# Optimization experiments

Hardware: AMD Instinct MI355X
Metric: run time of the kernel (lower is better)

Reference implementation:

```python
import jax, jax.numpy as jnp
from jax import lax
import numpy as np

B = 8
NC = 80               # num_classes / cls_out_channels
SCORE_THR = 0.01      # test_cfg.score_thr
IOU_THR = 0.65        # test_cfg.nms.iou_threshold
PRE_TOPK = 5000       # min(num_bboxes, 5000)
MAX_PER_IMG = 100     # keepTopK
LEVELS = [(80, 80, 8), (40, 40, 16), (20, 20, 32)]  # (H, W, stride)


def make_priors():
    # MlvlPointGenerator with_stride=True: [x*s, y*s, s, s]
    parts = []
    for H, W, s in LEVELS:
        ys, xs = jnp.meshgrid(jnp.arange(H, dtype=jnp.float32),
                              jnp.arange(W, dtype=jnp.float32), indexing='ij')
        st = jnp.full((H * W,), float(s), dtype=jnp.float32)
        parts.append(jnp.stack([xs.ravel() * s, ys.ravel() * s, st, st], -1))
    return jnp.concatenate(parts, 0)  # [N, 4]


def _flatten(t, c):
    # NCHW -> [B, H*W, c]
    return t.transpose(0, 2, 3, 1).reshape(t.shape[0], -1, c)


def _decode(priors, bp):
    # priors [N,4], bp [B,N,4] -> xyxy boxes [B,N,4]
    xys = bp[..., :2] * priors[:, 2:] + priors[:, :2]
    whs = jnp.exp(bp[..., 2:]) * priors[:, 2:]
    return jnp.concatenate([xys - whs / 2, xys + whs / 2], -1)


def _iou_one(box, boxes):
    # box [4] vs boxes [T,4]
    tl = jnp.maximum(box[:2], boxes[:, :2])
    br = jnp.minimum(box[2:], boxes[:, 2:])
    wh = jnp.clip(br - tl, 0.0)
    inter = wh[:, 0] * wh[:, 1]
    a1 = (box[2] - box[0]) * (box[3] - box[1])
    a2 = (boxes[:, 2] - boxes[:, 0]) * (boxes[:, 3] - boxes[:, 1])
    return inter / (a1 + a2 - inter + 1e-6)


def _nms_single(boxes, scores):
    # greedy NMS on one class: boxes [T,4], scores [T]
    s0 = jnp.where(scores > SCORE_THR, scores, -1.0)

    def step(s, _):
        i = jnp.argmax(s)
        best = s[i]
        iou = _iou_one(boxes[i], boxes)
        s = jnp.where(iou > IOU_THR, -1.0, s).at[i].set(-1.0)
        return s, (i, jnp.where(best > 0, best, -1.0))

    _, (idx, ks) = lax.scan(jax.checkpoint(step), s0, None, length=MAX_PER_IMG)
    return idx, ks  # [K] indices into boxes, [K] kept scores (-1 = invalid)


def _per_image(boxes, scores):
    # boxes [N,4], scores [N,C]
    top_s, top_i = lax.top_k(scores.T, PRE_TOPK)          # [C,T]
    top_b = boxes[top_i]                                   # [C,T,4]
    idx, ks = jax.vmap(_nms_single)(top_b, top_s)          # [C,K]
    cb = jnp.take_along_axis(top_b, idx[..., None], axis=1)  # [C,K,4]
    cids = jnp.broadcast_to(jnp.arange(NC, dtype=jnp.int32)[:, None], ks.shape)
    fs, sel = lax.top_k(ks.reshape(-1), MAX_PER_IMG)       # global keepTopK
    fb = cb.reshape(-1, 4)[sel]
    fc = cids.reshape(-1)[sel]
    valid = fs > 0
    num = jnp.sum(valid.astype(jnp.int32))
    return (num,
            jnp.where(valid[:, None], fb, 0.0),
            jnp.where(valid, fs, 0.0),
            jnp.where(valid, fc, -1))


def _forward(cls0, bbox0, obj0, cls1, bbox1, obj1, cls2, bbox2, obj2):
    cls = jnp.concatenate([_flatten(c, NC) for c in (cls0, cls1, cls2)], 1)
    bp = jnp.concatenate([_flatten(b, 4) for b in (bbox0, bbox1, bbox2)], 1)
    obj = jnp.concatenate([_flatten(o, 1)[..., 0] for o in (obj0, obj1, obj2)], 1)
    priors = make_priors()
    boxes = _decode(priors, bp)                            # [B,N,4]
    scores = jax.nn.sigmoid(cls) * jax.nn.sigmoid(obj)[..., None]  # [B,N,C]
    return jax.vmap(_per_image)(boxes, scores)


def setup_inputs() -> dict:
    key = jax.random.key(0)
    ks = jax.random.split(key, 9)
    specs = [("cls0", (B, NC, 80, 80)), ("bbox0", (B, 4, 80, 80)), ("obj0", (B, 1, 80, 80)),
             ("cls1", (B, NC, 40, 40)), ("bbox1", (B, 4, 40, 40)), ("obj1", (B, 1, 40, 40)),
             ("cls2", (B, NC, 20, 20)), ("bbox2", (B, 4, 20, 20)), ("obj2", (B, 1, 20, 20))]
    return {n: jax.random.normal(k, sh, dtype=jnp.float32) for k, (n, sh) in zip(ks, specs)}


def reference(cls0, bbox0, obj0, cls1, bbox1, obj1, cls2, bbox2, obj2):
    # returns (num_detected [B], proposals [B,100,4], scores [B,100], cls_id [B,100])
    return _forward(cls0, bbox0, obj0, cls1, bbox1, obj1, cls2, bbox2, obj2)
```

## Files before the change

kernel.cpp:

```cpp
#include <hip/hip_runtime.h>
#include <math.h>
#include <stdint.h>

#define NCLS   80
#define NPTS   8400
#define KEEP   100
#define PRETOPK 5000
#define NB     8
#define THRBITS 0x3C23D70Au
#define BASEK   0x3C000000u

#define TBS    512
#define CAPF   448
#define NEEDF  192u
#define MTX    256
#define NW4    2100

#define TBT    1024
#define NREGT  8
#define CAPT   512

__device__ __forceinline__ float sigmoidf_(float x) { return 1.0f / (1.0f + expf(-x)); }

__device__ __forceinline__ float4 decode_one(int n, int b,
        const float* bb0, const float* bb1, const float* bb2) {
    const float* bb; int base, HW, x, y; float s;
    if (n < 6400)      { bb = bb0; base = n;        HW = 6400; s = 8.f;  y = base / 80; x = base - y * 80; }
    else if (n < 8000) { bb = bb1; base = n - 6400; HW = 1600; s = 16.f; y = base / 40; x = base - y * 40; }
    else               { bb = bb2; base = n - 8000; HW = 400;  s = 32.f; y = base / 20; x = base - y * 20; }
    const float* p = bb + (size_t)b * 4 * HW + base;
    float v0 = p[0], v1 = p[HW], v2 = p[2 * HW], v3 = p[3 * HW];
    float cx = v0 * s + x * s, cy = v1 * s + y * s;
    float w = expf(v2) * s, h = expf(v3) * s;
    return make_float4(cx - 0.5f * w, cy - 0.5f * h, cx + 0.5f * w, cy + 0.5f * h);
}

__device__ __forceinline__ bool iou_gt(float4 a, float4 c) {
    float tlx = fmaxf(a.x, c.x), tly = fmaxf(a.y, c.y);
    float brx = fminf(a.z, c.z), bry = fminf(a.w, c.w);
    float w = fmaxf(brx - tlx, 0.f), h = fmaxf(bry - tly, 0.f);
    float inter = w * h;
    float a1 = (a.z - a.x) * (a.w - a.y);
    float a2 = (c.z - c.x) * (c.w - c.y);
    return inter / (a1 + a2 - inter + 1e-6f) > 0.65f;
}

__device__ __forceinline__ void scan_hist1024(const uint32_t* sHist, uint32_t need, uint32_t cap,
                                              uint32_t carry, uint32_t prefix, int shift,
                                              uint32_t* shr, int lane) {
    const uint4* hv = (const uint4*)sHist;
    uint4 q0 = hv[lane * 4], q1 = hv[lane * 4 + 1], q2 = hv[lane * 4 + 2], q3 = hv[lane * 4 + 3];
    uint32_t csum = q0.x + q0.y + q0.z + q0.w + q1.x + q1.y + q1.z + q1.w
                  + q2.x + q2.y + q2.z + q2.w + q3.x + q3.y + q3.z + q3.w;
    uint32_t suf = csum;
    #pragma unroll
    for (int d = 1; d < 64; d <<= 1) {
        uint32_t t = (uint32_t)__shfl_down((int)suf, d);
        if (lane + d < 64) suf += t;
    }
    unsigned long long m = __ballot(carry + suf >= need);
    if (!m) { if (lane == 0) { shr[1] = 0u; shr[0] = 0u; } return; }
    int l1 = 63 - __clzll(m);
    uint32_t carry2 = carry + (uint32_t)__shfl((int)suf, l1) - (uint32_t)__shfl((int)csum, l1);
    uint32_t c2 = (lane < 16) ? sHist[l1 * 16 + lane] : 0u;
    uint32_t suf2 = c2;
    #pragma unroll
    for (int d = 1; d < 16; d <<= 1) {
        uint32_t t = (uint32_t)__shfl_down((int)suf2, d);
        if (lane + d < 16) suf2 += t;
    }
    unsigned long long m2 = __ballot(lane < 16 && (carry2 + suf2 >= need));
    int t2 = m2 ? (63 - __clzll(m2)) : 0;
    uint32_t suf2L = (uint32_t)__shfl((int)suf2, t2);
    uint32_t c2L   = (uint32_t)__shfl((int)c2, t2);
    int bin = l1 * 16 + t2;
    uint32_t cAbove = carry2 + suf2L - c2L;
    uint32_t cntIncl = cAbove + c2L;
    if (lane == 0) {
        if (cntIncl <= cap) { shr[1] = 0u; shr[0] = prefix | ((uint32_t)bin << shift); }
        else { shr[1] = 1u; shr[2] = prefix | ((uint32_t)bin << shift); shr[3] = cAbove; }
    }
}

__device__ __forceinline__ void scan_hist64_final(const uint32_t* sHist, uint32_t need, uint32_t cap,
                                                  uint32_t carry, uint32_t prefix,
                                                  uint32_t* shr, int lane) {
    uint32_t c2 = sHist[lane];
    uint32_t suf2 = c2;
    #pragma unroll
    for (int d = 1; d < 64; d <<= 1) {
        uint32_t t = (uint32_t)__shfl_down((int)suf2, d);
        if (lane + d < 64) suf2 += t;
    }
    unsigned long long m2 = __ballot(carry + suf2 >= need);
    int t2 = m2 ? (63 - __clzll(m2)) : 0;
    uint32_t suf2L = (uint32_t)__shfl((int)suf2, t2);
    uint32_t c2L   = (uint32_t)__shfl((int)c2, t2);
    uint32_t cAbove = carry + suf2L - c2L;
    uint32_t cntIncl = cAbove + c2L;
    if (lane == 0) {
        shr[1] = 0u;
        shr[0] = (cntIncl <= cap) ? (prefix | (uint32_t)t2)
                                  : ((prefix | (uint32_t)t2) + 1u);
    }
}

__global__ __launch_bounds__(1024)
void sig_obj(const float* __restrict__ o0, const float* __restrict__ o1, const float* __restrict__ o2,
             float* __restrict__ so) {
    int t = blockIdx.x * 1024 + threadIdx.x;
    if (t >= NB * NPTS) return;
    int b = t / NPTS, n = t - b * NPTS;
    float v;
    if (n < 6400)      v = o0[(size_t)b * 6400 + n];
    else if (n < 8000) v = o1[(size_t)b * 1600 + (n - 6400)];
    else               v = o2[(size_t)b * 400 + (n - 8000)];
    so[t] = 1.0f / (1.0f + expf(-v));
}

__global__ __launch_bounds__(TBS, 6)
void select_nms(const float* __restrict__ cls0, const float* __restrict__ bb0,
                const float* __restrict__ cls1, const float* __restrict__ bb1,
                const float* __restrict__ cls2, const float* __restrict__ bb2,
                const float* __restrict__ sigObj,
                float* __restrict__ keptScore, float4* __restrict__ keptBox) {
    __shared__ __align__(16) uint32_t sKey[NPTS];
    __shared__ __align__(16) char uMem[8192];
    __shared__ uint32_t sKeyS[CAPF];
    __shared__ uint16_t sIdxS[CAPF];
    __shared__ __align__(16) float4 bBoxS[CAPF];
    __shared__ uint32_t shr[4];
    __shared__ unsigned long long sh64;

    uint32_t* sHist = (uint32_t*)uMem;
    unsigned long long* cPack = (unsigned long long*)(uMem + 4096);
    typedef unsigned long long ull4[4];
    ull4* colM = (ull4*)uMem;

    int bc = blockIdx.x;
    int b = bc & 7;
    int c = bc >> 3;
    int tid = threadIdx.x, lane = tid & 63;

    sHist[tid] = 0; sHist[tid + TBS] = 0;
    __syncthreads();
    uint4* sKey4 = (uint4*)sKey;
    #pragma unroll
    for (int i = 0; i < 5; ++i) {
        int w = tid + i * TBS;
        if (w < NW4) {
            int n = w << 2;
            const float* cp;
            if (w < 1600)      cp = cls0 + ((size_t)b * NCLS + c) * 6400 + n;
            else if (w < 2000) cp = cls1 + ((size_t)b * NCLS + c) * 1600 + (n - 6400);
            else               cp = cls2 + ((size_t)b * NCLS + c) * 400 + (n - 8000);
            float4 cv = *(const float4*)cp;
            float4 so = *(const float4*)(sigObj + (size_t)b * NPTS + n);
            uint32_t k0 = __float_as_uint(sigmoidf_(cv.x) * so.x);
            uint32_t k1 = __float_as_uint(sigmoidf_(cv.y) * so.y);
            uint32_t k2 = __float_as_uint(sigmoidf_(cv.z) * so.z);
            uint32_t k3 = __float_as_uint(sigmoidf_(cv.w) * so.w);
            sKey4[w] = make_uint4(k0, k1, k2, k3);
            if (k0 > THRBITS) atomicAdd(&sHist[(k0 - BASEK) >> 16], 1u);
            if (k1 > THRBITS) atomicAdd(&sHist[(k1 - BASEK) >> 16], 1u);
            if (k2 > THRBITS) atomicAdd(&sHist[(k2 - BASEK) >> 16], 1u);
            if (k3 > THRBITS) atomicAdd(&sHist[(k3 - BASEK) >> 16], 1u);
        }
    }
    __syncthreads();

    uint32_t prefix = 0, carry = 0, Tsel = 0;
    const uint4* k4 = (const uint4*)sKey;
    for (int level = 0;; ++level) {
        if (tid < 64) {
            if (level < 2) scan_hist1024(sHist, NEEDF, CAPF, carry, prefix, level == 0 ? 16 : 6, shr, lane);
            else           scan_hist64_final(sHist, NEEDF, CAPF, carry, prefix, shr, lane);
        }
        __syncthreads();
        if (shr[1] == 0u) { Tsel = shr[0]; break; }
        prefix = shr[2]; carry = shr[3];
        int nl = level + 1;
        if (nl == 2) { if (tid < 64) sHist[tid] = 0; } else { sHist[tid] = 0; sHist[tid + TBS] = 0; }
        __syncthreads();
        #pragma unroll
        for (int i = 0; i < 5; ++i) {
            int w = tid + i * TBS;
            if (w < NW4) {
                uint4 q = k4[w];
                #pragma unroll
                for (int j = 0; j < 4; ++j) {
                    uint32_t k = (j == 0) ? q.x : (j == 1) ? q.y : (j == 2) ? q.z : q.w;
                    if (k > THRBITS) {
                        uint32_t kp = k - BASEK;
                        if (nl == 1) { if ((kp >> 16) == (prefix >> 16)) atomicAdd(&sHist[(kp >> 6) & 1023u], 1u); }
                        else         { if ((kp >> 6)  == (prefix >> 6))  atomicAdd(&sHist[kp & 63u], 1u); }
                    }
                }
            }
        }
        __syncthreads();
    }
    __syncthreads();
    if (tid == 0) shr[3] = 0u;
    __syncthreads();

    #pragma unroll
    for (int i = 0; i < 5; ++i) {
        int w = tid + i * TBS;
        if (w < NW4) {
            uint4 q = k4[w];
            int n = w << 2;
            #pragma unroll
            for (int j = 0; j < 4; ++j) {
                uint32_t k = (j == 0) ? q.x : (j == 1) ? q.y : (j == 2) ? q.z : q.w;
                if (k > THRBITS && (k - BASEK) >= Tsel) {
                    uint32_t s = atomicAdd(&shr[3], 1u);
                    if (s < CAPF) cPack[s] = ((unsigned long long)k << 32) | (uint32_t)(0xFFFFu - (n + j));
                }
            }
        }
    }
    __syncthreads();
    int cnt = (int)shr[3]; if (cnt > CAPF) cnt = CAPF;
    if (tid < 16) cPack[cnt + tid] = 0ull;
    __syncthreads();

    if (tid < ((cnt + 63) & ~63)) {
        bool h0 = tid < cnt;
        unsigned long long my = h0 ? cPack[tid] : 0ull;
        int r0 = 0;
        const ulonglong2* cp2 = (const ulonglong2*)cPack;
        int nb16 = (cnt + 15) >> 4;
        for (int jb = 0; jb < nb16; ++jb) {
            ulonglong2 p0 = cp2[jb * 8 + 0], p1 = cp2[jb * 8 + 1], p2 = cp2[jb * 8 + 2], p3 = cp2[jb * 8 + 3];
            ulonglong2 p4 = cp2[jb * 8 + 4], p5 = cp2[jb * 8 + 5], p6 = cp2[jb * 8 + 6], p7 = cp2[jb * 8 + 7];
            r0 += (p0.x > my) + (p0.y > my) + (p1.x > my) + (p1.y > my)
                + (p2.x > my) + (p2.y > my) + (p3.x > my) + (p3.y > my)
                + (p4.x > my) + (p4.y > my) + (p5.x > my) + (p5.y > my)
                + (p6.x > my) + (p6.y > my) + (p7.x > my) + (p7.y > my);
        }
        if (h0) {
            sKeyS[r0] = (uint32_t)(my >> 32);
            sIdxS[r0] = (uint16_t)(0xFFFFu - (uint32_t)(my & 0xFFFFu));
        }
    }
    __syncthreads();

    if (tid < cnt) bBoxS[tid] = decode_one(sIdxS[tid], b, bb0, bb1, bb2);
    __syncthreads();

    int lim = (cnt < MTX) ? cnt : MTX;
    #pragma unroll
    for (int pp = 0; pp < 2; ++pp) {
        int t2 = tid + pp * TBS;
        int cand = t2 & 255, rb = t2 >> 8;
        unsigned long long m = 0ull;
        if (cand < lim) {
            float4 bcx = bBoxS[cand];
            int j0 = rb << 6;
            #pragma unroll 8
            for (int jj = 0; jj < 64; ++jj)
                if (iou_gt(bBoxS[j0 + jj], bcx)) m |= 1ull << jj;
        }
        colM[cand][rb] = m;
    }
    __syncthreads();

    float4 kb0 = make_float4(0.f, 0.f, 0.f, 0.f), kb1 = kb0;
    float ks0 = -1.0f, ks1 = -1.0f;
    int K = 0;
    if (tid < 64) {
        __builtin_amdgcn_s_setprio(1);
        unsigned long long U0, U1, U2, U3;
        U0 = (lim >= 64) ? ~0ull : ((lim > 0) ? ((1ull << lim) - 1) : 0ull);
        U1 = (lim >= 128) ? ~0ull : ((lim > 64) ? ((1ull << (lim - 64)) - 1) : 0ull);
        U2 = (lim >= 192) ? ~0ull : ((lim > 128) ? ((1ull << (lim - 128)) - 1) : 0ull);
        U3 = (lim >= 256) ? ~0ull : ((lim > 192) ? ((1ull << (lim - 192)) - 1) : 0ull);
        int kIA = -1, kIB = -1;
        while (K < KEEP) {
            int i;
            if (U0) i = (int)__ffsll(U0) - 1;
            else if (U1) i = 64 + (int)__ffsll(U1) - 1;
            else if (U2) i = 128 + (int)__ffsll(U2) - 1;
            else if (U3) i = 192 + (int)__ffsll(U3) - 1;
            else break;
            ulonglong2 r01 = *(const ulonglong2*)&colM[i][0];
            ulonglong2 r23 = *(const ulonglong2*)&colM[i][2];
            if (i < 64)       U0 &= ~(1ull << i);
            else if (i < 128) U1 &= ~(1ull << (i - 64));
            else if (i < 192) U2 &= ~(1ull << (i - 128));
            else              U3 &= ~(1ull << (i - 192));
            U0 &= ~r01.x; U1 &= ~r01.y; U2 &= ~r23.x; U3 &= ~r23.y;
            if (K < 64) { if (lane == K) kIA = i; }
            else        { if (lane == K - 64) kIB = i; }
            K++;
        }
        if (kIA >= 0) { kb0 = bBoxS[kIA]; ks0 = __uint_as_float(sKeyS[kIA]); }
        if (kIB >= 0) { kb1 = bBoxS[kIB]; ks1 = __uint_as_float(sKeyS[kIB]); }
        for (int i = lim; i < cnt && K < KEEP; ++i) {
            float4 bx = bBoxS[i];
            bool sup = false;
            if (lane < K)      sup = iou_gt(bx, kb0);
            if (64 + lane < K) sup = sup || iou_gt(bx, kb1);
            if (!__any(sup ? 1 : 0)) {
                float sc = __uint_as_float(sKeyS[i]);
                if (K < 64) { if (lane == K)      { kb0 = bx; ks0 = sc; } }
                else        { if (lane == K - 64) { kb1 = bx; ks1 = sc; } }
                K++;
            }
        }
        __builtin_amdgcn_s_setprio(0);
        if (lane == 0) {
            shr[0] = (uint32_t)K;
            shr[1] = (uint32_t)cnt;
            shr[2] = (cnt > 0) ? sKeyS[cnt - 1] : 0xFFFFFFFFu;
            shr[3] = (cnt > 0) ? (uint32_t)sIdxS[cnt - 1] : 0xFFFFFFFFu;
        }
    }
    __syncthreads();
    int Kall = (int)shr[0]; int e = (int)shr[1];
    uint32_t cK = shr[2], cI = shr[3];

    if (Kall < KEEP && e < PRETOPK) {
        for (;;) {
            if (tid == 0) sh64 = 0ull;
            __syncthreads();
            unsigned long long best = 0ull;
            for (int i = 0; i < 17; ++i) {
                int n = tid + i * TBS;
                if (n < NPTS) {
                    uint32_t k = sKey[n];
                    if (k > THRBITS && (k < cK || (k == cK && (uint32_t)n > cI))) {
                        unsigned long long v = ((unsigned long long)k << 32) | (unsigned long long)(NPTS - 1 - n);
                        if (v > best) best = v;
                    }
                }
            }
            if (best) atomicMax(&sh64, best);
            __syncthreads();
            unsigned long long bv = sh64;
            if (bv == 0ull) break;
            uint32_t k = (uint32_t)(bv >> 32);
            int n = NPTS - 1 - (int)(bv & 0xFFFFFFFFull);
            if (tid < 64) {
                float4 bx = decode_one(n, b, bb0, bb1, bb2);
                bool sup = false;
                if (lane < K)      sup = iou_gt(bx, kb0);
                if (64 + lane < K) sup = sup || iou_gt(bx, kb1);
                if (!__any(sup ? 1 : 0)) {
                    float sc = __uint_as_float(k);
                    if (K < 64) { if (lane == K)      { kb0 = bx; ks0 = sc; } }
                    else        { if (lane == K - 64) { kb1 = bx; ks1 = sc; } }
                    K++;
                }
                if (lane == 0) shr[0] = (uint32_t)K;
            }
            __syncthreads();
            Kall = (int)shr[0];
            e++; cK = k; cI = (uint32_t)n;
            if (Kall >= KEEP || e >= PRETOPK) break;
        }
    }

    if (tid < 64) {
        int off = (b * NCLS + c) * KEEP;
        float4 z = make_float4(0.f, 0.f, 0.f, 0.f);
        keptScore[off + lane] = (lane < K) ? ks0 : -1.0f;
        keptBox[off + lane]   = (lane < K) ? kb0 : z;
        if (64 + lane < KEEP) {
            keptScore[off + 64 + lane] = (64 + lane < K) ? ks1 : -1.0f;
            keptBox[off + 64 + lane]   = (64 + lane < K) ? kb1 : z;
        }
    }
}

__global__ __launch_bounds__(TBT)
void topk_out(const float* __restrict__ keptScore, const float4* __restrict__ keptBox,
              float* __restrict__ out) {
    __shared__ __align__(16) uint32_t sHist[1024];
    __shared__ __align__(16) unsigned long long cPackT[CAPT + 16];
    __shared__ uint32_t sKeyS[CAPT];
    __shared__ uint16_t sIdxS[CAPT];
    __shared__ uint32_t shr[4];
    int b = blockIdx.x, tid = threadIdx.x, lane = tid & 63;
    const int TOT = NCLS * KEEP;

    uint32_t rKey[NREGT];
    #pragma unroll
    for (int i = 0; i < NREGT; ++i) {
        int n = tid + i * TBT;
        uint32_t key = 0u;
        if (n < TOT) {
            float s = keptScore[b * TOT + n];
            key = (s > 0.f) ? __float_as_uint(s) : 0u;
        }
        rKey[i] = key;
    }

    uint32_t prefix = 0, carry = 0, Tsel = 0;
    for (int level = 0;; ++level) {
        __syncthreads();
        if (level == 2) { if (tid < 64) sHist[tid] = 0; } else sHist[tid] = 0;
        __syncthreads();
        #pragma unroll
        for (int i = 0; i < NREGT; ++i) {
            uint32_t k = rKey[i];
            if (k > 0u) {
                uint32_t kp = k - BASEK;
                if (level == 0) atomicAdd(&sHist[kp >> 16], 1u);
                else if (level == 1) { if ((kp >> 16) == (prefix >> 16)) atomicAdd(&sHist[(kp >> 6) & 1023u], 1u); }
                else { if ((kp >> 6) == (prefix >> 6)) atomicAdd(&sHist[kp & 63u], 1u); }
            }
        }
        __syncthreads();
        if (tid < 64) {
            if (level < 2) scan_hist1024(sHist, (uint32_t)KEEP, (uint32_t)CAPT, carry, prefix, level == 0 ? 16 : 6, shr, lane);
            else           scan_hist64_final(sHist, (uint32_t)KEEP, (uint32_t)CAPT, carry, prefix, shr, lane);
        }
        __syncthreads();
        if (shr[1] == 0u) { Tsel = shr[0]; break; }
        prefix = shr[2]; carry = shr[3];
    }
    __syncthreads();
    if (tid == 0) shr[3] = 0u;
    __syncthreads();
    #pragma unroll
    for (int i = 0; i < NREGT; ++i) {
        uint32_t k = rKey[i];
        if (k > 0u && (k - BASEK) >= Tsel) {
            uint32_t s = atomicAdd(&shr[3], 1u);
            if (s < CAPT) cPackT[s] = ((unsigned long long)k << 32) | (uint32_t)(0xFFFFu - (tid + i * TBT));
        }
    }
    __syncthreads();
    int cnt = (int)shr[3]; if (cnt > CAPT) cnt = CAPT;
    if (tid < 16) cPackT[cnt + tid] = 0ull;
    __syncthreads();

    if (tid < ((cnt + 63) & ~63)) {
        bool h0 = tid < cnt;
        unsigned long long my = h0 ? cPackT[tid] : 0ull;
        int r0 = 0;
        const ulonglong2* cp2 = (const ulonglong2*)cPackT;
        int nb16 = (cnt + 15) >> 4;
        for (int jb = 0; jb < nb16; ++jb) {
            ulonglong2 p0 = cp2[jb * 8 + 0], p1 = cp2[jb * 8 + 1], p2 = cp2[jb * 8 + 2], p3 = cp2[jb * 8 + 3];
            ulonglong2 p4 = cp2[jb * 8 + 4], p5 = cp2[jb * 8 + 5], p6 = cp2[jb * 8 + 6], p7 = cp2[jb * 8 + 7];
            r0 += (p0.x > my) + (p0.y > my) + (p1.x > my) + (p1.y > my)
                + (p2.x > my) + (p2.y > my) + (p3.x > my) + (p3.y > my)
                + (p4.x > my) + (p4.y > my) + (p5.x > my) + (p5.y > my)
                + (p6.x > my) + (p6.y > my) + (p7.x > my) + (p7.y > my);
        }
        if (h0) {
            sKeyS[r0] = (uint32_t)(my >> 32);
            sIdxS[r0] = (uint16_t)(0xFFFFu - (uint32_t)(my & 0xFFFFu));
        }
    }
    __syncthreads();

    if (tid < KEEP) {
        bool valid = tid < cnt;
        int fi = valid ? (int)sIdxS[tid] : 0;
        float sc = valid ? __uint_as_float(sKeyS[tid]) : 0.f;
        float4 bx = valid ? keptBox[b * TOT + fi] : make_float4(0.f, 0.f, 0.f, 0.f);
        float cls = valid ? (float)(fi / KEEP) : -1.0f;
        float* boxOut = out + NB + (b * KEEP + tid) * 4;
        boxOut[0] = bx.x; boxOut[1] = bx.y; boxOut[2] = bx.z; boxOut[3] = bx.w;
        out[NB + NB * KEEP * 4 + b * KEEP + tid] = sc;
        out[NB + NB * KEEP * 4 + NB * KEEP + b * KEEP + tid] = cls;
    }
    if (tid == 0) out[b] = (float)((cnt < KEEP) ? cnt : KEEP);
}

extern "C" void kernel_launch(void* const* d_in, const int* in_sizes, int n_in,
                              void* d_out, int out_size, void* d_ws, size_t ws_size,
                              hipStream_t stream) {
    const float* cls0 = (const float*)d_in[0];
    const float* bb0  = (const float*)d_in[1];
    const float* obj0 = (const float*)d_in[2];
    const float* cls1 = (const float*)d_in[3];
    const float* bb1  = (const float*)d_in[4];
    const float* obj1 = (const float*)d_in[5];
    const float* cls2 = (const float*)d_in[6];
    const float* bb2  = (const float*)d_in[7];
    const float* obj2 = (const float*)d_in[8];
    float* out = (float*)d_out;

    char* ws = (char*)d_ws;
    float*  keptScore = (float*)(ws);
    float4* keptBox   = (float4*)(ws + 256000);
    float*  sigObj    = (float*)(ws + 1280000);

    sig_obj<<<(NB * NPTS + 1023) / 1024, 1024, 0, stream>>>(obj0, obj1, obj2, sigObj);
    select_nms<<<NB * NCLS, TBS, 0, stream>>>(cls0, bb0, cls1, bb1, cls2, bb2,
                                              sigObj, keptScore, keptBox);
    topk_out<<<NB, TBT, 0, stream>>>(keptScore, keptBox, out);
}
```

Baseline: 159.3 us.

## Fuse objectness sigmoid into select kernel, triangular IoU mask, register-cached NMS rows

Drops the separate sig_obj launch and computes the objectness sigmoid inline from the raw obj inputs inside select_nms, so the per-class blocks recompute it rather than reading a precomputed buffer. The IoU bitmask build now skips blocks that lie entirely at or below the diagonal and masks out lower-triangle bits, roughly halving the pairwise IoU work. The serial greedy NMS loop preloads the suppression mask rows into registers and fetches them with wave shuffles instead of LDS reads on each iteration. The trade-offs are extra exp work per class block and higher register pressure in the NMS wave.

```diff
diff --git a/kernel.cpp b/kernel.cpp
--- a/kernel.cpp
+++ b/kernel.cpp
@@ -105,24 +105,13 @@
     }
 }
 
-__global__ __launch_bounds__(1024)
-void sig_obj(const float* __restrict__ o0, const float* __restrict__ o1, const float* __restrict__ o2,
-             float* __restrict__ so) {
-    int t = blockIdx.x * 1024 + threadIdx.x;
-    if (t >= NB * NPTS) return;
-    int b = t / NPTS, n = t - b * NPTS;
-    float v;
-    if (n < 6400)      v = o0[(size_t)b * 6400 + n];
-    else if (n < 8000) v = o1[(size_t)b * 1600 + (n - 6400)];
-    else               v = o2[(size_t)b * 400 + (n - 8000)];
-    so[t] = 1.0f / (1.0f + expf(-v));
-}
-
 __global__ __launch_bounds__(TBS, 6)
 void select_nms(const float* __restrict__ cls0, const float* __restrict__ bb0,
+                const float* __restrict__ o0,
                 const float* __restrict__ cls1, const float* __restrict__ bb1,
+                const float* __restrict__ o1,
                 const float* __restrict__ cls2, const float* __restrict__ bb2,
-                const float* __restrict__ sigObj,
+                const float* __restrict__ o2,
                 float* __restrict__ keptScore, float4* __restrict__ keptBox) {
     __shared__ __align__(16) uint32_t sKey[NPTS];
     __shared__ __align__(16) char uMem[8192];
@@ -150,16 +139,16 @@
         int w = tid + i * TBS;
         if (w < NW4) {
             int n = w << 2;
-            const float* cp;
-            if (w < 1600)      cp = cls0 + ((size_t)b * NCLS + c) * 6400 + n;
-            else if (w < 2000) cp = cls1 + ((size_t)b * NCLS + c) * 1600 + (n - 6400);
-            else               cp = cls2 + ((size_t)b * NCLS + c) * 400 + (n - 8000);
+            const float* cp; const float* op;
+            if (w < 1600)      { cp = cls0 + ((size_t)b * NCLS + c) * 6400 + n;          op = o0 + (size_t)b * 6400 + n; }
+            else if (w < 2000) { cp = cls1 + ((size_t)b * NCLS + c) * 1600 + (n - 6400); op = o1 + (size_t)b * 1600 + (n - 6400); }
+            else               { cp = cls2 + ((size_t)b * NCLS + c) * 400 + (n - 8000);  op = o2 + (size_t)b * 400 + (n - 8000); }
             float4 cv = *(const float4*)cp;
-            float4 so = *(const float4*)(sigObj + (size_t)b * NPTS + n);
-            uint32_t k0 = __float_as_uint(sigmoidf_(cv.x) * so.x);
-            uint32_t k1 = __float_as_uint(sigmoidf_(cv.y) * so.y);
-            uint32_t k2 = __float_as_uint(sigmoidf_(cv.z) * so.z);
-            uint32_t k3 = __float_as_uint(sigmoidf_(cv.w) * so.w);
+            float4 ov = *(const float4*)op;
+            uint32_t k0 = __float_as_uint(sigmoidf_(cv.x) * sigmoidf_(ov.x));
+            uint32_t k1 = __float_as_uint(sigmoidf_(cv.y) * sigmoidf_(ov.y));
+            uint32_t k2 = __float_as_uint(sigmoidf_(cv.z) * sigmoidf_(ov.z));
+            uint32_t k3 = __float_as_uint(sigmoidf_(cv.w) * sigmoidf_(ov.w));
             sKey4[w] = make_uint4(k0, k1, k2, k3);
             if (k0 > THRBITS) atomicAdd(&sHist[(k0 - BASEK) >> 16], 1u);
             if (k1 > THRBITS) atomicAdd(&sHist[(k1 - BASEK) >> 16], 1u);
@@ -254,13 +243,14 @@
     for (int pp = 0; pp < 2; ++pp) {
         int t2 = tid + pp * TBS;
         int cand = t2 & 255, rb = t2 >> 8;
+        int j0 = rb << 6;
         unsigned long long m = 0ull;
-        if (cand < lim) {
+        if (cand < lim && j0 + 63 > cand) {
             float4 bcx = bBoxS[cand];
-            int j0 = rb << 6;
             #pragma unroll 8
             for (int jj = 0; jj < 64; ++jj)
                 if (iou_gt(bBoxS[j0 + jj], bcx)) m |= 1ull << jj;
+            if (j0 <= cand) m &= ~((2ull << (cand - j0)) - 1ull);
         }
         colM[cand][rb] = m;
     }
@@ -270,6 +260,11 @@
     float ks0 = -1.0f, ks1 = -1.0f;
     int K = 0;
     if (tid < 64) {
+        const ulonglong2* cm2 = (const ulonglong2*)colM;
+        ulonglong2 a01 = cm2[lane * 2 + 0],        a23 = cm2[lane * 2 + 1];
+        ulonglong2 b01 = cm2[(64 + lane) * 2 + 0],  b23 = cm2[(64 + lane) * 2 + 1];
+        ulonglong2 c01 = cm2[(128 + lane) * 2 + 0], c23 = cm2[(128 + lane) * 2 + 1];
+        ulonglong2 d01 = cm2[(192 + lane) * 2 + 0], d23 = cm2[(192 + lane) * 2 + 1];
         __builtin_amdgcn_s_setprio(1);
         unsigned long long U0, U1, U2, U3;
         U0 = (lim >= 64) ? ~0ull : ((lim > 0) ? ((1ull << lim) - 1) : 0ull);
@@ -284,13 +279,17 @@
             else if (U2) i = 128 + (int)__ffsll(U2) - 1;
             else if (U3) i = 192 + (int)__ffsll(U3) - 1;
             else break;
-            ulonglong2 r01 = *(const ulonglong2*)&colM[i][0];
-            ulonglong2 r23 = *(const ulonglong2*)&colM[i][2];
+            int src = i & 63;
+            unsigned long long s0, s1, s2, s3;
+            if (i < 64)       { s0 = __shfl(a01.x, src); s1 = __shfl(a01.y, src); s2 = __shfl(a23.x, src); s3 = __shfl(a23.y, src); }
+            else if (i < 128) { s0 = __shfl(b01.x, src); s1 = __shfl(b01.y, src); s2 = __shfl(b23.x, src); s3 = __shfl(b23.y, src); }
+            else if (i < 192) { s0 = __shfl(c01.x, src); s1 = __shfl(c01.y, src); s2 = __shfl(c23.x, src); s3 = __shfl(c23.y, src); }
+            else              { s0 = __shfl(d01.x, src); s1 = __shfl(d01.y, src); s2 = __shfl(d23.x, src); s3 = __shfl(d23.y, src); }
             if (i < 64)       U0 &= ~(1ull << i);
             else if (i < 128) U1 &= ~(1ull << (i - 64));
             else if (i < 192) U2 &= ~(1ull << (i - 128));
             else              U3 &= ~(1ull << (i - 192));
-            U0 &= ~r01.x; U1 &= ~r01.y; U2 &= ~r23.x; U3 &= ~r23.y;
+            U0 &= ~s0; U1 &= ~s1; U2 &= ~s2; U3 &= ~s3;
             if (K < 64) { if (lane == K) kIA = i; }
             else        { if (lane == K - 64) kIB = i; }
             K++;
@@ -489,10 +488,8 @@
     char* ws = (char*)d_ws;
     float*  keptScore = (float*)(ws);
     float4* keptBox   = (float4*)(ws + 256000);
-    float*  sigObj    = (float*)(ws + 1280000);
-
-    sig_obj<<<(NB * NPTS + 1023) / 1024, 1024, 0, stream>>>(obj0, obj1, obj2, sigObj);
-    select_nms<<<NB * NCLS, TBS, 0, stream>>>(cls0, bb0, cls1, bb1, cls2, bb2,
-                                              sigObj, keptScore, keptBox);
+
+    select_nms<<<NB * NCLS, TBS, 0, stream>>>(cls0, bb0, obj0, cls1, bb1, obj1,
+                                              cls2, bb2, obj2, keptScore, keptBox);
     topk_out<<<NB, TBT, 0, stream>>>(keptScore, keptBox, out);
 }
```

Measured after the change: 165.2 us. +3.7%, slower.
